# Kernel optimization log

Hardware: AMD Instinct MI355X
Metric: run time of the kernel (lower is better)

Reference implementation:

```python
import jax, jax.numpy as jnp
import numpy as np


def setup_inputs() -> dict:
    key = jax.random.key(0)
    k1, k2 = jax.random.split(key)
    B, C, H, W = 16, 256, 64, 64
    K, D = 1024, 256
    z = jax.random.normal(k1, (B, C, H, W), dtype=jnp.float32)
    embedding = jax.random.normal(k2, (K, D), dtype=jnp.float32)
    return {"z": z, "embedding": embedding}


def reference(z, embedding):
    # _preprocess: shift channel dim (axis 1) to last, flatten -> [N, D]
    B, C, H, W = z.shape
    encoded_permuted = jnp.transpose(z, (0, 2, 3, 1))  # [B, H, W, C]
    permuted_shape = encoded_permuted.shape
    encoded_flat = encoded_permuted.reshape(-1, C)  # [N, D]

    x_sq = jnp.sum(encoded_flat * encoded_flat, axis=1, keepdims=True)  # [N, 1]
    e_sq = jnp.sum(embedding * embedding, axis=1)  # [K]
    cross = encoded_flat @ embedding.T  # [N, K]
    distances = x_sq - 2.0 * cross + e_sq[None, :]
    codebook_indices = jnp.argmin(distances, axis=1)  # [N]
    quantized_lookup = embedding[codebook_indices]  # [N, D]

    # straight-through estimator
    quantized_flat = encoded_flat + jax.lax.stop_gradient(quantized_lookup - encoded_flat)

    # _postprocess: reshape and shift last dim back to axis 1
    quantized = jnp.transpose(quantized_flat.reshape(permuted_shape), (0, 3, 1, 2))
    return (encoded_flat, quantized_flat, codebook_indices, quantized)
```

## Files before the change

kernel.cpp:

```cpp
#include <hip/hip_runtime.h>
#include <hip/hip_bf16.h>

typedef _Float16 h8 __attribute__((ext_vector_type(8)));
typedef float f4 __attribute__((ext_vector_type(4)));

#define N_TOK 65536
#define DIM 256
#define KCODES 1024
#define HWSZ 4096

__device__ __forceinline__ void gll16(const void* g, void* l) {
    __builtin_amdgcn_global_load_lds((const __attribute__((address_space(1))) void*)g,
                                     (__attribute__((address_space(3))) void*)l, 16, 0, 0);
}


__global__ void k_prep_frag(const float* __restrict__ emb, _Float16* __restrict__ BhF,
                            _Float16* __restrict__ BlF) {
    int gi = blockIdx.x * 256 + threadIdx.x;
    int kb = gi >> 9;
    int s = (gi >> 6) & 7;
    int dq = (gi >> 4) & 3;
    int r = gi & 15;
    int code = kb * 16 + r;
    int d0 = s * 32 + dq * 8;
    const float* src = emb + (size_t)code * DIM + d0;
    float4 x0 = *(const float4*)(src);
    float4 x1 = *(const float4*)(src + 4);
    float xs[8] = {x0.x, x0.y, x0.z, x0.w, x1.x, x1.y, x1.z, x1.w};
    h8 hi, lo;
#pragma unroll
    for (int j = 0; j < 8; ++j) {
        _Float16 h = (_Float16)xs[j];
        hi[j] = h;
        lo[j] = (_Float16)(xs[j] - (float)h);
    }
    *(h8*)(BhF + (size_t)gi * 8) = hi;
    *(h8*)(BlF + (size_t)gi * 8) = lo;
}

__global__ void k_esq(const float* __restrict__ emb, float* __restrict__ e_sq) {
    int t = threadIdx.x;
    int code = blockIdx.x * 4 + (t >> 6);
    int l = t & 63;
    float4 v = *(const float4*)(emb + (size_t)code * DIM + l * 4);
    float s = v.x * v.x + v.y * v.y + v.z * v.z + v.w * v.w;
#pragma unroll
    for (int off = 32; off >= 1; off >>= 1) s += __shfl_xor(s, off);
    if (l == 0) e_sq[code] = s;
}

__global__ void k_transpose(const float* __restrict__ z, float* __restrict__ enc,
                            _Float16* __restrict__ AhF, _Float16* __restrict__ AlF) {
    __shared__ float T[64][65];
    int blk = blockIdx.x;
    int b = blk >> 8;
    int rem = blk & 255;
    int c0 = (rem >> 6) * 64;
    int hw0 = (rem & 63) * 64;
    int t = threadIdx.x;
    const float* zp = z + (size_t)b * DIM * HWSZ;
    {
        int hw4 = (t & 15) * 4, cl = t >> 4;
#pragma unroll
        for (int i = 0; i < 4; ++i) {
            int c = cl + i * 16;
            float4 v = *(const float4*)(zp + (size_t)(c0 + c) * HWSZ + hw0 + hw4);
            T[c][hw4 + 0] = v.x; T[c][hw4 + 1] = v.y;
            T[c][hw4 + 2] = v.z; T[c][hw4 + 3] = v.w;
        }
    }
    __syncthreads();
    {
        int c4 = (t & 15) * 4, hwl = t >> 4;
#pragma unroll
        for (int i = 0; i < 4; ++i) {
            int hw = hwl + i * 16;
            float4 v;
            v.x = T[c4 + 0][hw]; v.y = T[c4 + 1][hw];
            v.z = T[c4 + 2][hw]; v.w = T[c4 + 3][hw];
            *(float4*)(enc + (size_t)(b * HWSZ + hw0 + hw) * DIM + c0 + c4) = v;
        }
    }
    {
        int base_nb = b * 256 + (hw0 >> 4);
#pragma unroll
        for (int i = 0; i < 2; ++i) {
            int gidx = i * 256 + t;
            int nbi = gidx >> 7;
            int si = (gidx >> 6) & 1;
            int dq = (gidx >> 4) & 3;
            int r = gidx & 15;
            int hwl = nbi * 16 + r;
            int cl = si * 32 + dq * 8;
            h8 hi, lo;
#pragma unroll
            for (int j = 0; j < 8; ++j) {
                float x = T[cl + j][hwl];
                _Float16 h = (_Float16)x;
                hi[j] = h;
                lo[j] = (_Float16)(x - (float)h);
            }
            size_t G = (((size_t)(base_nb + nbi) * 8) + (c0 >> 5) + si) * 64 + dq * 16 + r;
            *(h8*)(AhF + G * 8) = hi;
            *(h8*)(AlF + G * 8) = lo;
        }
    }
}

#define WAITV(n) asm volatile("s_waitcnt vmcnt(" #n ")" ::: "memory")
#define BARRIER __builtin_amdgcn_s_barrier()

__global__ __launch_bounds__(512)
void k_gemm_argmin(const _Float16* __restrict__ AhF, const _Float16* __restrict__ AlF,
                   const _Float16* __restrict__ BhF, const _Float16* __restrict__ BlF,
                   const float* __restrict__ e_sq,
                   float* __restrict__ pV1, int* __restrict__ pI1) {
    __shared__ _Float16 S[49152];

    int gid = blockIdx.x;
    int colTile = gid >> 9, rowTile = gid & 511;
    int r0 = rowTile * 128, c0 = colTile * 256;
    int t = threadIdx.x;
    int w = t >> 6, l = t & 63;
    int wm = w >> 2, wn = w & 3;
    int l16 = l & 15, lhi = l >> 4;

    const char* gAh = (const char*)AhF + (((size_t)(rowTile * 8 + w)) << 13) + (l << 4);
    const char* gAl = (const char*)AlF + (((size_t)(rowTile * 8 + w)) << 13) + (l << 4);
    const char* gBh0 = (const char*)BhF + (((size_t)(colTile * 16 + w)) << 13) + (l << 4);
    const char* gBh1 = gBh0 + (8ll << 13);
    const char* gBl0 = (const char*)BlF + (((size_t)(colTile * 16 + w)) << 13) + (l << 4);
    const char* gBl1 = gBl0 + (8ll << 13);

    char* SB = (char*)S;
    int aOff = w << 10;
    int bOff0 = 8192 + (w << 10);
    int bOff1 = 8192 + ((8 + w) << 10);

#define ISSUE_H(s, b) do { int so = (s) << 10; char* bp = SB + (b) * 24576; \
    gll16(gAh + so, bp + aOff); gll16(gBh0 + so, bp + bOff0); gll16(gBh1 + so, bp + bOff1); } while (0)
#define ISSUE_L(s, b) do { int so = (s) << 10; char* bp = SB + (b) * 24576; \
    gll16(gAl + so, bp + aOff); gll16(gBl0 + so, bp + bOff0); gll16(gBl1 + so, bp + bOff1); } while (0)
#define READ_A(b, dst) do { const char* bp = SB + (b) * 24576; \
    _Pragma("unroll") for (int mf = 0; mf < 4; ++mf) \
        dst[mf] = *(const h8*)(bp + (((wm * 4 + mf) << 10) + (l << 4))); } while (0)
#define READ_B(b, dst) do { const char* bp = SB + (b) * 24576 + 8192; \
    _Pragma("unroll") for (int nf = 0; nf < 4; ++nf) \
        dst[nf] = *(const h8*)(bp + (((wn * 4 + nf) << 10) + (l << 4))); } while (0)
#define MFMA16(A_, B_) do { _Pragma("unroll") for (int mf = 0; mf < 4; ++mf) \
    _Pragma("unroll") for (int nf = 0; nf < 4; ++nf) \
        acc[mf][nf] = __builtin_amdgcn_mfma_f32_16x16x32_f16(A_[mf], B_[nf], acc[mf][nf], 0, 0, 0); } while (0)
#define PRIO1 __builtin_amdgcn_s_setprio(1)
#define PRIO0 __builtin_amdgcn_s_setprio(0)

    f4 acc[4][4];
#pragma unroll
    for (int i = 0; i < 4; ++i)
#pragma unroll
        for (int j = 0; j < 4; ++j) acc[i][j] = (f4)0.0f;

    h8 ah[4], bh[4], al[4], bl[4];

    ISSUE_H(0, 0); ISSUE_L(0, 1); ISSUE_H(1, 2);

    for (int s = 0; s < 6; s += 2) {
        WAITV(6); BARRIER; ISSUE_L(s + 1, 3); READ_A(0, ah); READ_B(0, bh);
        PRIO1; MFMA16(ah, bh); PRIO0;
        WAITV(6); BARRIER; ISSUE_H(s + 2, 0); READ_A(1, al); READ_B(1, bl);
        PRIO1; MFMA16(ah, bl); MFMA16(al, bh); PRIO0;
        WAITV(6); BARRIER; ISSUE_L(s + 2, 1); READ_A(2, ah); READ_B(2, bh);
        PRIO1; MFMA16(ah, bh); PRIO0;
        WAITV(6); BARRIER; ISSUE_H(s + 3, 2); READ_A(3, al); READ_B(3, bl);
        PRIO1; MFMA16(ah, bl); MFMA16(al, bh); PRIO0;
    }
    WAITV(6); BARRIER; ISSUE_L(7, 3); READ_A(0, ah); READ_B(0, bh);
    PRIO1; MFMA16(ah, bh); PRIO0;
    WAITV(6); BARRIER; READ_A(1, al); READ_B(1, bl);
    PRIO1; MFMA16(ah, bl); MFMA16(al, bh); PRIO0;
    WAITV(3); BARRIER; READ_A(2, ah); READ_B(2, bh);
    PRIO1; MFMA16(ah, bh); PRIO0;
    WAITV(0); BARRIER; READ_A(3, al); READ_B(3, bl);
    PRIO1; MFMA16(ah, bl); MFMA16(al, bh); PRIO0;

    float* smV = (float*)S;
    int* smI = (int*)S + 512;

    float esq[4];
#pragma unroll
    for (int nf = 0; nf < 4; ++nf) esq[nf] = e_sq[c0 + wn * 64 + nf * 16 + l16];

#pragma unroll
    for (int mf = 0; mf < 4; ++mf) {
#pragma unroll
        for (int rg = 0; rg < 4; ++rg) {
            float bestV = 3.4e38f;
            int bestI = 0;
#pragma unroll
            for (int nf = 0; nf < 4; ++nf) {
                float v = esq[nf] - 2.0f * acc[mf][nf][rg];
                int ci = c0 + wn * 64 + nf * 16 + l16;
                if (v < bestV || (v == bestV && ci < bestI)) { bestV = v; bestI = ci; }
            }
#pragma unroll
            for (int off = 1; off < 16; off <<= 1) {
                float vv = __shfl_xor(bestV, off);
                int ii = __shfl_xor(bestI, off);
                if (vv < bestV || (vv == bestV && ii < bestI)) { bestV = vv; bestI = ii; }
            }
            if (l16 == 0) {
                int rloc = wm * 64 + mf * 16 + lhi * 4 + rg;
                smV[wn * 128 + rloc] = bestV;
                smI[wn * 128 + rloc] = bestI;
            }
        }
    }
    __syncthreads();
    if (t < 128) {
        float bestV = smV[t];
        int bestI = smI[t];
#pragma unroll
        for (int wn2 = 1; wn2 < 4; ++wn2) {
            float v = smV[wn2 * 128 + t];
            int i2 = smI[wn2 * 128 + t];
            if (v < bestV || (v == bestV && i2 < bestI)) { bestV = v; bestI = i2; }
        }
        pV1[colTile * N_TOK + r0 + t] = bestV;
        pI1[colTile * N_TOK + r0 + t] = bestI;
    }
}

__global__ void k_final_out1(const float* __restrict__ pV1, const int* __restrict__ pI1,
                             const float* __restrict__ emb,
                             float* __restrict__ out2, int* __restrict__ idxI,
                             float* __restrict__ out1) {
    __shared__ int sidx[256];
    int t = threadIdx.x;
    int n0 = blockIdx.x * 256;
    int n = n0 + t;
    float v1 = pV1[n];
    int i1 = pI1[n];
#pragma unroll
    for (int ct = 1; ct < 4; ++ct) {
        float a1 = pV1[ct * N_TOK + n];
        int ai = pI1[ct * N_TOK + n];
        if (a1 < v1 || (a1 == v1 && ai < i1)) { v1 = a1; i1 = ai; }
    }
    out2[n] = (float)i1;
    idxI[n] = i1;
    sidx[t] = i1;
    __syncthreads();
    int rr = t >> 2, q = t & 3;
#pragma unroll
    for (int i = 0; i < 4; ++i) {
        int r = i * 64 + rr;
        int idx = sidx[r];
        const float* src = emb + (size_t)idx * DIM + q * 64;
        float* dst = out1 + (size_t)(n0 + r) * DIM + q * 64;
#pragma unroll
        for (int j = 0; j < 16; ++j)
            *(float4*)(dst + j * 4) = *(const float4*)(src + j * 4);
    }
}

__global__ void k_out3(const float* __restrict__ emb, const int* __restrict__ idxI,
                       float* __restrict__ out3) {
    __shared__ float E[32][257];
    int blk = blockIdx.x;
    int b = blk >> 7, hwt = blk & 127;
    int hw0 = hwt * 32;
    int n0 = b * HWSZ + hw0;
    int t = threadIdx.x;
    {
        int r = t >> 3, oct = t & 7;
        int idx = idxI[n0 + r];
        const float* src = emb + (size_t)idx * DIM + oct * 32;
#pragma unroll
        for (int i = 0; i < 8; ++i) {
            float4 v = *(const float4*)(src + i * 4);
            E[r][oct * 32 + i * 4 + 0] = v.x;
            E[r][oct * 32 + i * 4 + 1] = v.y;
            E[r][oct * 32 + i * 4 + 2] = v.z;
            E[r][oct * 32 + i * 4 + 3] = v.w;
        }
    }
    __syncthreads();
    {
        int w = t >> 6, l = t & 63;
        int ch = l >> 5, hw = l & 31;
        float* dst = out3 + (size_t)b * DIM * HWSZ + hw0 + hw;
#pragma unroll
        for (int it = 0; it < 32; ++it) {
            int c = w * 64 + it * 2 + ch;
            dst[(size_t)c * HWSZ] = E[hw][c];
        }
    }
}

extern "C" void kernel_launch(void* const* d_in, const int* in_sizes, int n_in,
                              void* d_out, int out_size, void* d_ws, size_t ws_size,
                              hipStream_t stream) {
    const float* z = (const float*)d_in[0];
    const float* emb = (const float*)d_in[1];
    float* out = (float*)d_out;
    float* out0 = out;
    float* out1 = out + 16777216;
    float* out2 = out + 33554432;
    float* out3 = out + 33619968;

    _Float16* AhF = (_Float16*)out1;
    _Float16* AlF = (_Float16*)(out1 + 8388608);

    char* ws = (char*)d_ws;
    _Float16* BhF = (_Float16*)(ws);
    _Float16* BlF = (_Float16*)(ws + 524288);
    float* e_sq = (float*)(ws + 1048576);
    float* pV1 = (float*)(ws + 1052672);
    int* pI1 = (int*)(ws + 2101248);
    int* idxI = (int*)(ws + 3149824);

    k_prep_frag<<<128, 256, 0, stream>>>(emb, BhF, BlF);
    k_esq<<<256, 256, 0, stream>>>(emb, e_sq);
    k_transpose<<<4096, 256, 0, stream>>>(z, out0, AhF, AlF);
    k_gemm_argmin<<<2048, 512, 0, stream>>>(AhF, AlF, BhF, BlF, e_sq, pV1, pI1);
    k_final_out1<<<256, 256, 0, stream>>>(pV1, pI1, emb, out2, idxI, out1);
    k_out3<<<2048, 256, 0, stream>>>(emb, idxI, out3);
}
```

Before: 254.5 us.

## Use 16-wave blocks with six-stage LDS pipeline and grouped tile order

The GEMM-argmin kernel goes from 8 to 16 waves per block, each computing a 32x64 sub-tile instead of 64x64, while only the first 8 waves issue global-to-LDS loads. The LDS ring grows from 4 to 6 buffers (dynamic shared memory, 144 KB) with five loads in flight, and block IDs are remapped so blocks sharing a row chunk and all four column tiles run close together for better L2 reuse. The aim is more latency hiding and MFMA overlap. In exchange each block uses far more LDS, which limits residency to one block per CU, and more barriers are shared across more waves.

```diff
diff --git a/kernel.cpp b/kernel.cpp
--- a/kernel.cpp
+++ b/kernel.cpp
@@ -110,16 +110,20 @@
 
 #define WAITV(n) asm volatile("s_waitcnt vmcnt(" #n ")" ::: "memory")
 #define BARRIER __builtin_amdgcn_s_barrier()
-
-__global__ __launch_bounds__(512)
+#define PRIO1 __builtin_amdgcn_s_setprio(1)
+#define PRIO0 __builtin_amdgcn_s_setprio(0)
+
+extern __shared__ char SB[];
+
+__global__ __launch_bounds__(1024)
 void k_gemm_argmin(const _Float16* __restrict__ AhF, const _Float16* __restrict__ AlF,
                    const _Float16* __restrict__ BhF, const _Float16* __restrict__ BlF,
                    const float* __restrict__ e_sq,
                    float* __restrict__ pV1, int* __restrict__ pI1) {
-    __shared__ _Float16 S[49152];
-
     int gid = blockIdx.x;
-    int colTile = gid >> 9, rowTile = gid & 511;
+    int rchunk = gid >> 8;
+    int colTile = (gid >> 6) & 3;
+    int rowTile = rchunk * 64 + (gid & 63);
     int r0 = rowTile * 128, c0 = colTile * 256;
     int t = threadIdx.x;
     int w = t >> 6, l = t & 63;
@@ -128,70 +132,68 @@
 
     const char* gAh = (const char*)AhF + (((size_t)(rowTile * 8 + w)) << 13) + (l << 4);
     const char* gAl = (const char*)AlF + (((size_t)(rowTile * 8 + w)) << 13) + (l << 4);
-    const char* gBh0 = (const char*)BhF + (((size_t)(colTile * 16 + w)) << 13) + (l << 4);
-    const char* gBh1 = gBh0 + (8ll << 13);
-    const char* gBl0 = (const char*)BlF + (((size_t)(colTile * 16 + w)) << 13) + (l << 4);
-    const char* gBl1 = gBl0 + (8ll << 13);
-
-    char* SB = (char*)S;
-    int aOff = w << 10;
-    int bOff0 = 8192 + (w << 10);
-    int bOff1 = 8192 + ((8 + w) << 10);
-
-#define ISSUE_H(s, b) do { int so = (s) << 10; char* bp = SB + (b) * 24576; \
-    gll16(gAh + so, bp + aOff); gll16(gBh0 + so, bp + bOff0); gll16(gBh1 + so, bp + bOff1); } while (0)
-#define ISSUE_L(s, b) do { int so = (s) << 10; char* bp = SB + (b) * 24576; \
-    gll16(gAl + so, bp + aOff); gll16(gBl0 + so, bp + bOff0); gll16(gBl1 + so, bp + bOff1); } while (0)
-#define READ_A(b, dst) do { const char* bp = SB + (b) * 24576; \
-    _Pragma("unroll") for (int mf = 0; mf < 4; ++mf) \
-        dst[mf] = *(const h8*)(bp + (((wm * 4 + mf) << 10) + (l << 4))); } while (0)
-#define READ_B(b, dst) do { const char* bp = SB + (b) * 24576 + 8192; \
+    const char* gBh0 = (const char*)BhF + (((size_t)(colTile * 16 + 2 * w)) << 13) + (l << 4);
+    const char* gBh1 = gBh0 + (1ll << 13);
+    const char* gBl0 = (const char*)BlF + (((size_t)(colTile * 16 + 2 * w)) << 13) + (l << 4);
+    const char* gBl1 = gBl0 + (1ll << 13);
+
+#define ISSUE_P(p) do { \
+    const int s_ = (p) >> 1, buf_ = (p) % 6; \
+    const char* a_ = ((p) & 1) ? gAl : gAh; \
+    const char* b0_ = ((p) & 1) ? gBl0 : gBh0; \
+    const char* b1_ = ((p) & 1) ? gBl1 : gBh1; \
+    char* bp_ = SB + buf_ * 24576; \
+    gll16(a_ + (s_ << 10), bp_ + (w << 10)); \
+    gll16(b0_ + (s_ << 10), bp_ + 8192 + ((2 * w) << 10)); \
+    gll16(b1_ + (s_ << 10), bp_ + 8192 + ((2 * w + 1) << 10)); \
+} while (0)
+
+#define READ_A(buf, dst) { const char* bp_ = SB + (buf) * 24576; \
+    _Pragma("unroll") for (int mf = 0; mf < 2; ++mf) \
+        dst[mf] = *(const h8*)(bp_ + ((wm * 2 + mf) << 10) + (l << 4)); }
+#define READ_B(buf, dst) { const char* bp_ = SB + (buf) * 24576 + 8192; \
     _Pragma("unroll") for (int nf = 0; nf < 4; ++nf) \
-        dst[nf] = *(const h8*)(bp + (((wn * 4 + nf) << 10) + (l << 4))); } while (0)
-#define MFMA16(A_, B_) do { _Pragma("unroll") for (int mf = 0; mf < 4; ++mf) \
+        dst[nf] = *(const h8*)(bp_ + ((wn * 4 + nf) << 10) + (l << 4)); }
+#define MFMA8(A_, B_) { _Pragma("unroll") for (int mf = 0; mf < 2; ++mf) \
     _Pragma("unroll") for (int nf = 0; nf < 4; ++nf) \
-        acc[mf][nf] = __builtin_amdgcn_mfma_f32_16x16x32_f16(A_[mf], B_[nf], acc[mf][nf], 0, 0, 0); } while (0)
-#define PRIO1 __builtin_amdgcn_s_setprio(1)
-#define PRIO0 __builtin_amdgcn_s_setprio(0)
-
-    f4 acc[4][4];
-#pragma unroll
-    for (int i = 0; i < 4; ++i)
+        acc[mf][nf] = __builtin_amdgcn_mfma_f32_16x16x32_f16(A_[mf], B_[nf], acc[mf][nf], 0, 0, 0); }
+
+#define PHASE(q, W, DO_ISSUE) \
+    if (w < 8) { WAITV(W); } \
+    BARRIER; \
+    if ((DO_ISSUE) && w < 8) { ISSUE_P((q) + 5); } \
+    if (((q) & 1) == 0) { \
+        READ_A((q) % 6, ah); READ_B((q) % 6, bh); \
+        PRIO1; MFMA8(ah, bh); PRIO0; \
+    } else { \
+        READ_A((q) % 6, al); READ_B((q) % 6, bl); \
+        PRIO1; MFMA8(ah, bl); MFMA8(al, bh); PRIO0; \
+    }
+
+    f4 acc[2][4];
+#pragma unroll
+    for (int i = 0; i < 2; ++i)
 #pragma unroll
         for (int j = 0; j < 4; ++j) acc[i][j] = (f4)0.0f;
 
-    h8 ah[4], bh[4], al[4], bl[4];
-
-    ISSUE_H(0, 0); ISSUE_L(0, 1); ISSUE_H(1, 2);
-
-    for (int s = 0; s < 6; s += 2) {
-        WAITV(6); BARRIER; ISSUE_L(s + 1, 3); READ_A(0, ah); READ_B(0, bh);
-        PRIO1; MFMA16(ah, bh); PRIO0;
-        WAITV(6); BARRIER; ISSUE_H(s + 2, 0); READ_A(1, al); READ_B(1, bl);
-        PRIO1; MFMA16(ah, bl); MFMA16(al, bh); PRIO0;
-        WAITV(6); BARRIER; ISSUE_L(s + 2, 1); READ_A(2, ah); READ_B(2, bh);
-        PRIO1; MFMA16(ah, bh); PRIO0;
-        WAITV(6); BARRIER; ISSUE_H(s + 3, 2); READ_A(3, al); READ_B(3, bl);
-        PRIO1; MFMA16(ah, bl); MFMA16(al, bh); PRIO0;
-    }
-    WAITV(6); BARRIER; ISSUE_L(7, 3); READ_A(0, ah); READ_B(0, bh);
-    PRIO1; MFMA16(ah, bh); PRIO0;
-    WAITV(6); BARRIER; READ_A(1, al); READ_B(1, bl);
-    PRIO1; MFMA16(ah, bl); MFMA16(al, bh); PRIO0;
-    WAITV(3); BARRIER; READ_A(2, ah); READ_B(2, bh);
-    PRIO1; MFMA16(ah, bh); PRIO0;
-    WAITV(0); BARRIER; READ_A(3, al); READ_B(3, bl);
-    PRIO1; MFMA16(ah, bl); MFMA16(al, bh); PRIO0;
-
-    float* smV = (float*)S;
-    int* smI = (int*)S + 512;
+    h8 ah[2], al[2], bh[4], bl[4];
+
+    if (w < 8) { ISSUE_P(0); ISSUE_P(1); ISSUE_P(2); ISSUE_P(3); ISSUE_P(4); }
+
+    PHASE(0, 12, 1)  PHASE(1, 12, 1)  PHASE(2, 12, 1)  PHASE(3, 12, 1)
+    PHASE(4, 12, 1)  PHASE(5, 12, 1)  PHASE(6, 12, 1)  PHASE(7, 12, 1)
+    PHASE(8, 12, 1)  PHASE(9, 12, 1)  PHASE(10, 12, 1) PHASE(11, 12, 0)
+    PHASE(12, 9, 0)  PHASE(13, 6, 0)  PHASE(14, 3, 0)  PHASE(15, 0, 0)
+
+    float* smV = (float*)SB;
+    int* smI = (int*)(SB + 2048);
 
     float esq[4];
 #pragma unroll
     for (int nf = 0; nf < 4; ++nf) esq[nf] = e_sq[c0 + wn * 64 + nf * 16 + l16];
 
 #pragma unroll
-    for (int mf = 0; mf < 4; ++mf) {
+    for (int mf = 0; mf < 2; ++mf) {
 #pragma unroll
         for (int rg = 0; rg < 4; ++rg) {
             float bestV = 3.4e38f;
@@ -209,7 +211,7 @@
                 if (vv < bestV || (vv == bestV && ii < bestI)) { bestV = vv; bestI = ii; }
             }
             if (l16 == 0) {
-                int rloc = wm * 64 + mf * 16 + lhi * 4 + rg;
+                int rloc = wm * 32 + mf * 16 + lhi * 4 + rg;
                 smV[wn * 128 + rloc] = bestV;
                 smI[wn * 128 + rloc] = bestI;
             }
@@ -319,10 +321,17 @@
     int* pI1 = (int*)(ws + 2101248);
     int* idxI = (int*)(ws + 3149824);
 
+    static bool attr_set = false;
+    if (!attr_set) {
+        hipFuncSetAttribute((const void*)k_gemm_argmin,
+                            hipFuncAttributeMaxDynamicSharedMemorySize, 147456);
+        attr_set = true;
+    }
+
     k_prep_frag<<<128, 256, 0, stream>>>(emb, BhF, BlF);
     k_esq<<<256, 256, 0, stream>>>(emb, e_sq);
     k_transpose<<<4096, 256, 0, stream>>>(z, out0, AhF, AlF);
-    k_gemm_argmin<<<2048, 512, 0, stream>>>(AhF, AlF, BhF, BlF, e_sq, pV1, pI1);
+    k_gemm_argmin<<<2048, 1024, 147456, stream>>>(AhF, AlF, BhF, BlF, e_sq, pV1, pI1);
     k_final_out1<<<256, 256, 0, stream>>>(pV1, pI1, emb, out2, idxI, out1);
     k_out3<<<2048, 256, 0, stream>>>(emb, idxI, out3);
 }
```

New measurement: 209.9 us. -17.5%, faster.
